# Optimization experiments

Hardware: AMD Instinct MI355X
Metric: run time of the kernel (lower is better)

Reference implementation:

```python
import jax, jax.numpy as jnp
import numpy as np

B, L, D, C, NB = 2, 256, 3, 256, 64
LN_EPS = 1e-5


def setup_inputs() -> dict:
    ks = jax.random.split(jax.random.key(0), 12)
    x_BLD = jax.random.normal(ks[0], (B, L, D), dtype=jnp.float32) * 0.5
    c_BD = jax.random.normal(ks[1], (B, C), dtype=jnp.float32)
    embed_w = jax.random.normal(ks[2], (NB, C), dtype=jnp.float32) * 0.02
    pos_w = jax.random.normal(ks[3], (128, C), dtype=jnp.float32) * 0.02
    bins = jnp.linspace(0.0, 3.0, NB - 1, dtype=jnp.float32)
    ada_w = jax.random.normal(ks[4], (3 * C, C), dtype=jnp.float32) * (C ** -0.5)
    ada_b = jnp.zeros((3 * C,), dtype=jnp.float32)
    ln_g = jnp.ones((C,), dtype=jnp.float32)
    ln_b = jnp.zeros((C,), dtype=jnp.float32)
    fc1_w = jax.random.normal(ks[5], (4 * C, C), dtype=jnp.float32) * (C ** -0.5)
    fc1_b = jnp.zeros((4 * C,), dtype=jnp.float32)
    fc2_w = jax.random.normal(ks[6], (C, 4 * C), dtype=jnp.float32) * ((4 * C) ** -0.5)
    fc2_b = jnp.zeros((C,), dtype=jnp.float32)
    return {"x_BLD": x_BLD, "c_BD": c_BD, "embed_w": embed_w, "pos_w": pos_w,
            "bins": bins, "ada_w": ada_w, "ada_b": ada_b, "ln_g": ln_g,
            "ln_b": ln_b, "fc1_w": fc1_w, "fc1_b": fc1_b, "fc2_w": fc2_w,
            "fc2_b": fc2_b}


def reference(x_BLD, c_BD, embed_w, pos_w, bins, ada_w, ada_b, ln_g, ln_b,
              fc1_w, fc1_b, fc2_w, fc2_b):
    # pairwise squared distances: [B, L, L]
    d_BLL = jnp.sum((x_BLD[:, :, None, :] - x_BLD[:, None, :, :]) ** 2, axis=-1)
    # bucketize (torch.bucketize right=False == searchsorted side='left')
    idx_BLL = jnp.searchsorted(bins, d_BLL, side="left")
    # relative position embedding: [L, L, C]
    rel = jnp.arange(L)[:, None] - jnp.arange(L)[None, :]
    rel = jnp.clip(rel, -64, 63) + 64
    pos_LLD = pos_w[rel]
    # adaLN modulation from conditioning: SiLU -> Linear -> 3 chunks
    mod = jax.nn.silu(c_BD) @ ada_w.T + ada_b            # [B, 3C]
    shift, scale, gate = jnp.split(mod, 3, axis=-1)      # each [B, C]
    shift = shift[:, None, None, :]
    scale = scale[:, None, None, :]
    gate = gate[:, None, None, :]
    # embed + pos, affine modulate
    s = embed_w[idx_BLL] + pos_LLD[None]                 # [B, L, L, C]
    s = s * (1.0 + scale) + shift
    # LayerNorm over channel dim
    mu = jnp.mean(s, axis=-1, keepdims=True)
    var = jnp.mean((s - mu) ** 2, axis=-1, keepdims=True)
    h = (s - mu) * jax.lax.rsqrt(var + LN_EPS) * ln_g + ln_b
    # MLP: Linear -> GELU(exact) -> Linear
    h = jax.nn.gelu(h @ fc1_w.T + fc1_b, approximate=False)
    h = h @ fc2_w.T + fc2_b
    return s + gate * h
```

## Files before the change

### kernel.cpp

```cpp
#include <hip/hip_runtime.h>
#include <math.h>

#define Cn 256
#define Ln 256
#define Bn 2
#define ROWS 8
#define H1 1024
#define NIDX 64
#define NREL 128
#define NCOMBO (Bn * NIDX * NREL)
#define TROWS 32

typedef __attribute__((ext_vector_type(8))) short bf16x8;
typedef __attribute__((ext_vector_type(4))) float f32x4;

__device__ __forceinline__ float gelu_exact(float x) {
    return 0.5f * x * (1.0f + erff(x * 0.70710678118654752f));
}

__device__ __forceinline__ short f2bf(float f) {
    unsigned u = __float_as_uint(f);
    unsigned r = (u + 0x7fffu + ((u >> 16) & 1u)) >> 16;
    return (short)r;
}

__global__ __launch_bounds__(256) void mod_kernel(
    const float* __restrict__ c_BD, const float* __restrict__ ada_w,
    const float* __restrict__ ada_b, float* __restrict__ mod)
{
    int o = blockIdx.x * 256 + threadIdx.x;
    int b = o / (3 * Cn);
    int j = o - b * (3 * Cn);
    const float* crow = c_BD + b * Cn;
    const float* wrow = ada_w + (size_t)j * Cn;
    float acc = 0.f;
    for (int k = 0; k < Cn; k += 4) {
        float4 cv = *(const float4*)(crow + k);
        float4 wv = *(const float4*)(wrow + k);
        acc += (cv.x / (1.f + expf(-cv.x))) * wv.x;
        acc += (cv.y / (1.f + expf(-cv.y))) * wv.y;
        acc += (cv.z / (1.f + expf(-cv.z))) * wv.z;
        acc += (cv.w / (1.f + expf(-cv.w))) * wv.w;
    }
    mod[o] = acc + ada_b[j];
}

__global__ __launch_bounds__(256) void cvt_kernel(
    const float* __restrict__ s, short* __restrict__ d, int n)
{
    int i = (blockIdx.x * 256 + threadIdx.x) * 4;
    if (i < n) {
        float4 v = *(const float4*)(s + i);
        short4 o;
        o.x = f2bf(v.x); o.y = f2bf(v.y); o.z = f2bf(v.z); o.w = f2bf(v.w);
        *(short4*)(d + i) = o;
    }
}

__global__ __launch_bounds__(256) void table_mfma_kernel(
    const float* __restrict__ embed_w, const float* __restrict__ pos_w,
    const float* __restrict__ ln_g, const float* __restrict__ ln_b,
    const short* __restrict__ fc1bf, const float* __restrict__ fc1_b,
    const short* __restrict__ fc2bf, const float* __restrict__ fc2_b,
    const float* __restrict__ mod, float* __restrict__ table)
{
    __shared__ __align__(16) short h_lds[TROWS][264];
    __shared__ __align__(16) short g_lds[TROWS][264];
    __shared__ float s_lds[TROWS][260];

    const int tid  = threadIdx.x;
    const int wave = tid >> 6;
    const int lane = tid & 63;
    const int quad = lane >> 4;
    const int l15  = lane & 15;

    const int base = blockIdx.x * TROWS;
    const int b    = base >> 13;
    const int idx  = (base >> 7) & 63;
    const int rel0 = base & 127;

    const float* modb = mod + b * (3 * Cn);
    const float* erow = embed_w + (size_t)idx * Cn;

    float scale[4], shift[4], lng[4], lnb[4], ev[4];
    #pragma unroll
    for (int m = 0; m < 4; ++m) {
        int c = lane + 64 * m;
        scale[m] = 1.f + modb[Cn + c];
        shift[m] = modb[c];
        lng[m]   = ln_g[c];
        lnb[m]   = ln_b[c];
        ev[m]    = erow[c];
    }

    for (int r8 = 0; r8 < 8; ++r8) {
        const int rr = wave * 8 + r8;
        const float* prow = pos_w + (size_t)(rel0 + rr) * Cn;
        float sv[4]; float sum = 0.f;
        #pragma unroll
        for (int m = 0; m < 4; ++m) {
            float v = (ev[m] + prow[lane + 64 * m]) * scale[m] + shift[m];
            sv[m] = v; sum += v;
        }
        #pragma unroll
        for (int off = 32; off; off >>= 1) sum += __shfl_xor(sum, off, 64);
        float mu = sum * (1.f / Cn);
        float p2 = 0.f;
        #pragma unroll
        for (int m = 0; m < 4; ++m) { float t = sv[m] - mu; p2 += t * t; }
        #pragma unroll
        for (int off = 32; off; off >>= 1) p2 += __shfl_xor(p2, off, 64);
        float rstd = rsqrtf(p2 * (1.f / Cn) + 1e-5f);
        #pragma unroll
        for (int m = 0; m < 4; ++m) {
            int c = lane + 64 * m;
            s_lds[rr][c] = sv[m];
            h_lds[rr][c] = f2bf((sv[m] - mu) * rstd * lng[m] + lnb[m]);
        }
    }
    __syncthreads();

    f32x4 acc2[2][4];
    #pragma unroll
    for (int mt = 0; mt < 2; ++mt)
        #pragma unroll
        for (int nt = 0; nt < 4; ++nt) acc2[mt][nt] = (f32x4){0.f, 0.f, 0.f, 0.f};

    for (int c = 0; c < 4; ++c) {
        f32x4 z[2][4];
        #pragma unroll
        for (int mt = 0; mt < 2; ++mt)
            #pragma unroll
            for (int nt = 0; nt < 4; ++nt) z[mt][nt] = (f32x4){0.f, 0.f, 0.f, 0.f};

        #pragma unroll
        for (int ks = 0; ks < 8; ++ks) {
            int k0 = ks * 32 + quad * 8;
            bf16x8 a0 = *(const bf16x8*)(&h_lds[l15][k0]);
            bf16x8 a1 = *(const bf16x8*)(&h_lds[16 + l15][k0]);
            #pragma unroll
            for (int nt = 0; nt < 4; ++nt) {
                int n = c * 256 + wave * 64 + nt * 16 + l15;
                bf16x8 bf = *(const bf16x8*)(fc1bf + (size_t)n * Cn + k0);
                z[0][nt] = __builtin_amdgcn_mfma_f32_16x16x32_bf16(a0, bf, z[0][nt], 0, 0, 0);
                z[1][nt] = __builtin_amdgcn_mfma_f32_16x16x32_bf16(a1, bf, z[1][nt], 0, 0, 0);
            }
        }
        __syncthreads();
        #pragma unroll
        for (int mt = 0; mt < 2; ++mt)
            #pragma unroll
            for (int nt = 0; nt < 4; ++nt) {
                int coll = wave * 64 + nt * 16 + l15;
                float bias = fc1_b[c * 256 + coll];
                #pragma unroll
                for (int r = 0; r < 4; ++r) {
                    int row = mt * 16 + quad * 4 + r;
                    g_lds[row][coll] = f2bf(gelu_exact(z[mt][nt][r] + bias));
                }
            }
        __syncthreads();
        #pragma unroll
        for (int ks = 0; ks < 8; ++ks) {
            int k0 = ks * 32 + quad * 8;
            bf16x8 a0 = *(const bf16x8*)(&g_lds[l15][k0]);
            bf16x8 a1 = *(const bf16x8*)(&g_lds[16 + l15][k0]);
            #pragma unroll
            for (int nt = 0; nt < 4; ++nt) {
                int n = wave * 64 + nt * 16 + l15;
                bf16x8 bf = *(const bf16x8*)(fc2bf + (size_t)n * H1 + c * 256 + k0);
                acc2[0][nt] = __builtin_amdgcn_mfma_f32_16x16x32_bf16(a0, bf, acc2[0][nt], 0, 0, 0);
                acc2[1][nt] = __builtin_amdgcn_mfma_f32_16x16x32_bf16(a1, bf, acc2[1][nt], 0, 0, 0);
            }
        }
    }

    #pragma unroll
    for (int nt = 0; nt < 4; ++nt) {
        int col = wave * 64 + nt * 16 + l15;
        float bias = fc2_b[col];
        float gate = modb[2 * Cn + col];
        #pragma unroll
        for (int mt = 0; mt < 2; ++mt)
            #pragma unroll
            for (int r = 0; r < 4; ++r) {
                int row = mt * 16 + quad * 4 + r;
                float v = acc2[mt][nt][r] + bias;
                table[(size_t)(base + row) * Cn + col] = s_lds[row][col] + gate * v;
            }
    }
}

__global__ __launch_bounds__(256) void gather_kernel(
    const float* __restrict__ x, const float* __restrict__ bins,
    const float* __restrict__ table, float* __restrict__ out)
{
    __shared__ float xs[Ln * 3];
    __shared__ float bins_s[63];
    __shared__ int   idx_s[64];

    const int tid = threadIdx.x;
    const int blk = blockIdx.x;
    const int q   = blk & 3;
    const int bi  = blk >> 2;
    const int b   = bi >> 8;
    const int i   = bi & 255;

    for (int t = tid; t < Ln * 3; t += 256) xs[t] = x[(size_t)b * Ln * 3 + t];
    if (tid < 63) bins_s[tid] = bins[tid];
    __syncthreads();

    if (tid < 64) {
        int j = q * 64 + tid;
        float d0 = xs[3 * i]     - xs[3 * j];
        float d1 = xs[3 * i + 1] - xs[3 * j + 1];
        float d2 = xs[3 * i + 2] - xs[3 * j + 2];
        float d = d0 * d0 + d1 * d1 + d2 * d2;
        int v = 0;
        #pragma unroll
        for (int k = 0; k < 63; ++k) v += (bins_s[k] < d) ? 1 : 0;
        idx_s[tid] = v;
    }
    __syncthreads();

    const int wave = tid >> 6;
    const int lane = tid & 63;
    float4* outp = (float4*)(out + (size_t)bi * Ln * Cn);
    const float4* tab4 = (const float4*)table;

    #pragma unroll 4
    for (int jj = 0; jj < 16; ++jj) {
        int jl = wave * 16 + jj;
        int j  = q * 64 + jl;
        int idx = idx_s[jl];
        int rel = i - j;
        rel = (rel < -64 ? -64 : (rel > 63 ? 63 : rel)) + 64;
        size_t trow = (size_t)((b * NIDX + idx) * NREL + rel) * (Cn / 4);
        outp[(size_t)j * (Cn / 4) + lane] = tab4[trow + lane];
    }
}

__global__ __launch_bounds__(256) void table_kernel(
    const float* __restrict__ embed_w, const float* __restrict__ pos_w,
    const float* __restrict__ ln_g, const float* __restrict__ ln_b,
    const float* __restrict__ fc1_w, const float* __restrict__ fc1_b,
    const float* __restrict__ fc2_w, const float* __restrict__ fc2_b,
    const float* __restrict__ mod, float* __restrict__ table)
{
    __shared__ float s_tile[ROWS][Cn];
    __shared__ float h_tile[ROWS][Cn];
    __shared__ float g_tile[ROWS][H1];

    const int tid  = threadIdx.x;
    const int wave = tid >> 6;
    const int lane = tid & 63;

    const int base = blockIdx.x * ROWS;
    const int b    = base >> 13;
    const int idx  = (base >> 7) & 63;
    const int rel0 = base & 127;

    const float* modb = mod + b * (3 * Cn);
    const float* erow = embed_w + (size_t)idx * Cn;

    for (int rr = wave; rr < ROWS; rr += 4) {
        const float* prow = pos_w + (size_t)(rel0 + rr) * Cn;
        float sv[4]; float partial = 0.f;
        #pragma unroll
        for (int m = 0; m < 4; ++m) {
            const int c = lane + 64 * m;
            const float v = (erow[c] + prow[c]) * (1.f + modb[Cn + c]) + modb[c];
            sv[m] = v; partial += v;
        }
        float sum = partial;
        #pragma unroll
        for (int off = 32; off; off >>= 1) sum += __shfl_xor(sum, off, 64);
        const float mu = sum * (1.f / Cn);
        float p2 = 0.f;
        #pragma unroll
        for (int m = 0; m < 4; ++m) { const float t = sv[m] - mu; p2 += t * t; }
        float vs = p2;
        #pragma unroll
        for (int off = 32; off; off >>= 1) vs += __shfl_xor(vs, off, 64);
        const float rstd = rsqrtf(vs * (1.f / Cn) + 1e-5f);
        #pragma unroll
        for (int m = 0; m < 4; ++m) {
            const int c = lane + 64 * m;
            s_tile[rr][c] = sv[m];
            h_tile[rr][c] = (sv[m] - mu) * rstd * ln_g[c] + ln_b[c];
        }
    }
    __syncthreads();

    {
        float acc[ROWS][4];
        #pragma unroll
        for (int r = 0; r < ROWS; ++r)
            #pragma unroll
            for (int m = 0; m < 4; ++m) acc[r][m] = 0.f;

        const float* w0 = fc1_w + (size_t)(4 * tid + 0) * Cn;
        const float* w1 = fc1_w + (size_t)(4 * tid + 1) * Cn;
        const float* w2 = fc1_w + (size_t)(4 * tid + 2) * Cn;
        const float* w3 = fc1_w + (size_t)(4 * tid + 3) * Cn;

        for (int k = 0; k < Cn; k += 4) {
            const float4 a0 = *(const float4*)(w0 + k);
            const float4 a1 = *(const float4*)(w1 + k);
            const float4 a2 = *(const float4*)(w2 + k);
            const float4 a3 = *(const float4*)(w3 + k);
            #pragma unroll
            for (int r = 0; r < ROWS; ++r) {
                const float4 h4 = *(const float4*)(&h_tile[r][k]);
                acc[r][0] += h4.x * a0.x + h4.y * a0.y + h4.z * a0.z + h4.w * a0.w;
                acc[r][1] += h4.x * a1.x + h4.y * a1.y + h4.z * a1.z + h4.w * a1.w;
                acc[r][2] += h4.x * a2.x + h4.y * a2.y + h4.z * a2.z + h4.w * a2.w;
                acc[r][3] += h4.x * a3.x + h4.y * a3.y + h4.z * a3.z + h4.w * a3.w;
            }
        }
        const float b0 = fc1_b[4 * tid + 0];
        const float b1 = fc1_b[4 * tid + 1];
        const float b2 = fc1_b[4 * tid + 2];
        const float b3 = fc1_b[4 * tid + 3];
        #pragma unroll
        for (int r = 0; r < ROWS; ++r) {
            float4 g;
            g.x = gelu_exact(acc[r][0] + b0);
            g.y = gelu_exact(acc[r][1] + b1);
            g.z = gelu_exact(acc[r][2] + b2);
            g.w = gelu_exact(acc[r][3] + b3);
            *(float4*)(&g_tile[r][4 * tid]) = g;
        }
    }
    __syncthreads();

    {
        float acc2[ROWS];
        #pragma unroll
        for (int r = 0; r < ROWS; ++r) acc2[r] = 0.f;

        const float* w2r = fc2_w + (size_t)tid * H1;
        for (int k = 0; k < H1; k += 4) {
            const float4 wv = *(const float4*)(w2r + k);
            #pragma unroll
            for (int r = 0; r < ROWS; ++r) {
                const float4 g = *(const float4*)(&g_tile[r][k]);
                acc2[r] += g.x * wv.x + g.y * wv.y + g.z * wv.z + g.w * wv.w;
            }
        }
        const float bias = fc2_b[tid];
        const float gate = modb[2 * Cn + tid];
        #pragma unroll
        for (int r = 0; r < ROWS; ++r)
            table[(size_t)(base + r) * Cn + tid] = s_tile[r][tid] + gate * (acc2[r] + bias);
    }
}

__global__ __launch_bounds__(256) void main_kernel_fb(
    const float* __restrict__ x, const float* __restrict__ embed_w,
    const float* __restrict__ pos_w, const float* __restrict__ bins,
    const float* __restrict__ ln_g, const float* __restrict__ ln_b,
    const float* __restrict__ fc1_w, const float* __restrict__ fc1_b,
    const float* __restrict__ fc2_w, const float* __restrict__ fc2_b,
    const float* __restrict__ mod, float* __restrict__ out)
{
    __shared__ float s_tile[ROWS][Cn];
    __shared__ float h_tile[ROWS][Cn];
    __shared__ float g_tile[ROWS][H1];
    __shared__ float bins_s[64];

    const int tid  = threadIdx.x;
    const int wave = tid >> 6;
    const int lane = tid & 63;

    const long base = (long)blockIdx.x * ROWS;
    const int  b    = (int)(base / (Ln * Ln));
    const int  rem  = (int)(base % (Ln * Ln));
    const int  i    = rem / Ln;
    const int  j0   = rem % Ln;

    if (tid < 63) bins_s[tid] = bins[tid];
    __syncthreads();

    const float* xi = x + ((long)b * Ln + i) * 3;
    const float xi0 = xi[0], xi1 = xi[1], xi2 = xi[2];
    const float* modb = mod + b * (3 * Cn);

    for (int rr = wave; rr < ROWS; rr += 4) {
        const int j = j0 + rr;
        const float* xj = x + ((long)b * Ln + j) * 3;
        const float d0 = xi0 - xj[0], d1 = xi1 - xj[1], d2 = xi2 - xj[2];
        const float d = d0 * d0 + d1 * d1 + d2 * d2;
        int idx = 0;
        #pragma unroll
        for (int k = 0; k < 63; ++k) idx += (bins_s[k] < d) ? 1 : 0;
        int rel = i - j;
        rel = (rel < -64 ? -64 : (rel > 63 ? 63 : rel)) + 64;
        const float* erow = embed_w + (size_t)idx * Cn;
        const float* prow = pos_w + (size_t)rel * Cn;

        float sv[4]; float partial = 0.f;
        #pragma unroll
        for (int m = 0; m < 4; ++m) {
            const int c = lane + 64 * m;
            const float v = (erow[c] + prow[c]) * (1.f + modb[Cn + c]) + modb[c];
            sv[m] = v; partial += v;
        }
        float sum = partial;
        #pragma unroll
        for (int off = 32; off; off >>= 1) sum += __shfl_xor(sum, off, 64);
        const float mu = sum * (1.f / Cn);
        float p2 = 0.f;
        #pragma unroll
        for (int m = 0; m < 4; ++m) { const float t = sv[m] - mu; p2 += t * t; }
        float vs = p2;
        #pragma unroll
        for (int off = 32; off; off >>= 1) vs += __shfl_xor(vs, off, 64);
        const float rstd = rsqrtf(vs * (1.f / Cn) + 1e-5f);
        #pragma unroll
        for (int m = 0; m < 4; ++m) {
            const int c = lane + 64 * m;
            s_tile[rr][c] = sv[m];
            h_tile[rr][c] = (sv[m] - mu) * rstd * ln_g[c] + ln_b[c];
        }
    }
    __syncthreads();

    {
        float acc[ROWS][4];
        #pragma unroll
        for (int r = 0; r < ROWS; ++r)
            #pragma unroll
            for (int m = 0; m < 4; ++m) acc[r][m] = 0.f;

        const float* w0 = fc1_w + (size_t)(4 * tid + 0) * Cn;
        const float* w1 = fc1_w + (size_t)(4 * tid + 1) * Cn;
        const float* w2 = fc1_w + (size_t)(4 * tid + 2) * Cn;
        const float* w3 = fc1_w + (size_t)(4 * tid + 3) * Cn;

        for (int k = 0; k < Cn; k += 4) {
            const float4 a0 = *(const float4*)(w0 + k);
            const float4 a1 = *(const float4*)(w1 + k);
            const float4 a2 = *(const float4*)(w2 + k);
            const float4 a3 = *(const float4*)(w3 + k);
            #pragma unroll
            for (int r = 0; r < ROWS; ++r) {
                const float4 h4 = *(const float4*)(&h_tile[r][k]);
                acc[r][0] += h4.x * a0.x + h4.y * a0.y + h4.z * a0.z + h4.w * a0.w;
                acc[r][1] += h4.x * a1.x + h4.y * a1.y + h4.z * a1.z + h4.w * a1.w;
                acc[r][2] += h4.x * a2.x + h4.y * a2.y + h4.z * a2.z + h4.w * a2.w;
                acc[r][3] += h4.x * a3.x + h4.y * a3.y + h4.z * a3.z + h4.w * a3.w;
            }
        }
        const float b0 = fc1_b[4 * tid + 0];
        const float b1 = fc1_b[4 * tid + 1];
        const float b2 = fc1_b[4 * tid + 2];
        const float b3 = fc1_b[4 * tid + 3];
        #pragma unroll
        for (int r = 0; r < ROWS; ++r) {
            float4 g;
            g.x = gelu_exact(acc[r][0] + b0);
            g.y = gelu_exact(acc[r][1] + b1);
            g.z = gelu_exact(acc[r][2] + b2);
            g.w = gelu_exact(acc[r][3] + b3);
            *(float4*)(&g_tile[r][4 * tid]) = g;
        }
    }
    __syncthreads();

    {
        float acc2[ROWS];
        #pragma unroll
        for (int r = 0; r < ROWS; ++r) acc2[r] = 0.f;

        const float* w2r = fc2_w + (size_t)tid * H1;
        for (int k = 0; k < H1; k += 4) {
            const float4 wv = *(const float4*)(w2r + k);
            #pragma unroll
            for (int r = 0; r < ROWS; ++r) {
                const float4 g = *(const float4*)(&g_tile[r][k]);
                acc2[r] += g.x * wv.x + g.y * wv.y + g.z * wv.z + g.w * wv.w;
            }
        }
        const float bias = fc2_b[tid];
        const float gate = modb[2 * Cn + tid];
        #pragma unroll
        for (int r = 0; r < ROWS; ++r)
            out[(base + r) * Cn + tid] = s_tile[r][tid] + gate * (acc2[r] + bias);
    }
}

extern "C" void kernel_launch(void* const* d_in, const int* in_sizes, int n_in,
                              void* d_out, int out_size, void* d_ws, size_t ws_size,
                              hipStream_t stream) {
    const float* x_BLD   = (const float*)d_in[0];
    const float* c_BD    = (const float*)d_in[1];
    const float* embed_w = (const float*)d_in[2];
    const float* pos_w   = (const float*)d_in[3];
    const float* bins    = (const float*)d_in[4];
    const float* ada_w   = (const float*)d_in[5];
    const float* ada_b   = (const float*)d_in[6];
    const float* ln_g    = (const float*)d_in[7];
    const float* ln_b    = (const float*)d_in[8];
    const float* fc1_w   = (const float*)d_in[9];
    const float* fc1_b   = (const float*)d_in[10];
    const float* fc2_w   = (const float*)d_in[11];
    const float* fc2_b   = (const float*)d_in[12];
    float* out = (float*)d_out;

    float* mod   = (float*)d_ws;
    short* fc1bf = (short*)((char*)d_ws + 8192);
    short* fc2bf = fc1bf + Cn * H1;
    float* table = (float*)((char*)d_ws + 8192 + 2 * Cn * H1 * sizeof(short));

    const size_t need3 = 8192 + 2 * (size_t)Cn * H1 * sizeof(short)
                       + (size_t)NCOMBO * Cn * sizeof(float);
    const size_t need2 = 8192 + (size_t)NCOMBO * Cn * sizeof(float);

    mod_kernel<<<(Bn * 3 * Cn) / 256, 256, 0, stream>>>(c_BD, ada_w, ada_b, mod);

    if (ws_size >= need3) {
        cvt_kernel<<<(Cn * H1 / 4 + 255) / 256, 256, 0, stream>>>(fc1_w, fc1bf, Cn * H1);
        cvt_kernel<<<(Cn * H1 / 4 + 255) / 256, 256, 0, stream>>>(fc2_w, fc2bf, Cn * H1);
        table_mfma_kernel<<<NCOMBO / TROWS, 256, 0, stream>>>(
            embed_w, pos_w, ln_g, ln_b, fc1bf, fc1_b, fc2bf, fc2_b, mod, table);
        gather_kernel<<<Bn * Ln * 4, 256, 0, stream>>>(x_BLD, bins, table, out);
    } else if (ws_size >= need2) {
        float* table2 = (float*)((char*)d_ws + 8192);
        table_kernel<<<NCOMBO / ROWS, 256, 0, stream>>>(
            embed_w, pos_w, ln_g, ln_b, fc1_w, fc1_b, fc2_w, fc2_b, mod, table2);
        gather_kernel<<<Bn * Ln * 4, 256, 0, stream>>>(x_BLD, bins, table2, out);
    } else {
        main_kernel_fb<<<(Bn * Ln * Ln) / ROWS, 256, 0, stream>>>(
            x_BLD, embed_w, pos_w, bins, ln_g, ln_b,
            fc1_w, fc1_b, fc2_w, fc2_b, mod, out);
    }
}
```

Measured before the change: 280.7 us.

## Split table MLP into LN kernel plus two tiled MFMA GEMMs with async LDS loads

Replaces the fused per-32-row table kernel with three stages: a LayerNorm kernel writing bf16 h and fp32 s, a 128x128-tiled bf16 MFMA GEMM for fc1 with fused GELU, and a 64x128-tiled GEMM for fc2 with the fused gate and residual epilogue. Tiles are staged into LDS through global_load_lds async copies, and the gather kernel now issues all 16 loads before its stores. The aim is better weight reuse and MFMA utilisation than the small-row fused kernel. In exchange it writes and reads large intermediate buffers (h, s and the GELU output) through global memory and needs about 76 MB of workspace, falling back to the old fused kernel when less is available.

```diff
diff --git a/kernel.cpp b/kernel.cpp
--- a/kernel.cpp
+++ b/kernel.cpp
@@ -4,24 +4,27 @@
 #define Cn 256
 #define Ln 256
 #define Bn 2
-#define ROWS 8
 #define H1 1024
 #define NIDX 64
 #define NREL 128
-#define NCOMBO (Bn * NIDX * NREL)
+#define NCOMBO 16384
+#define BK 64
 #define TROWS 32
 
 typedef __attribute__((ext_vector_type(8))) short bf16x8;
 typedef __attribute__((ext_vector_type(4))) float f32x4;
+typedef unsigned int u32;
 
 __device__ __forceinline__ float gelu_exact(float x) {
     return 0.5f * x * (1.0f + erff(x * 0.70710678118654752f));
 }
-
 __device__ __forceinline__ short f2bf(float f) {
     unsigned u = __float_as_uint(f);
-    unsigned r = (u + 0x7fffu + ((u >> 16) & 1u)) >> 16;
-    return (short)r;
+    return (short)((u + 0x7fffu + ((u >> 16) & 1u)) >> 16);
+}
+__device__ __forceinline__ void async16(const void* g, void* l) {
+    __builtin_amdgcn_global_load_lds((const __attribute__((address_space(1))) u32*)g,
+                                     (__attribute__((address_space(3))) u32*)l, 16, 0, 0);
 }
 
 __global__ __launch_bounds__(256) void mod_kernel(
@@ -57,6 +60,258 @@
     }
 }
 
+__global__ __launch_bounds__(256) void ln_kernel(
+    const float* __restrict__ embed_w, const float* __restrict__ pos_w,
+    const float* __restrict__ ln_g, const float* __restrict__ ln_b,
+    const float* __restrict__ mod,
+    float* __restrict__ s_out, short* __restrict__ h_out)
+{
+    const int tid  = threadIdx.x;
+    const int wave = tid >> 6;
+    const int lane = tid & 63;
+    const int base = blockIdx.x * 8;
+    const int b    = base >> 13;
+    const int idx  = (base >> 7) & 63;
+    const int rel0 = base & 127;
+    const float* modb = mod + b * (3 * Cn);
+    const int c0 = lane * 4;
+
+    const float4 ev = *(const float4*)(embed_w + (size_t)idx * Cn + c0);
+    const float4 sc = *(const float4*)(modb + Cn + c0);
+    const float4 sh = *(const float4*)(modb + c0);
+    const float4 lg = *(const float4*)(ln_g + c0);
+    const float4 lb = *(const float4*)(ln_b + c0);
+
+    #pragma unroll
+    for (int r8 = 0; r8 < 2; ++r8) {
+        const int rr  = wave * 2 + r8;
+        const int row = base + rr;
+        const float4 p = *(const float4*)(pos_w + (size_t)(rel0 + rr) * Cn + c0);
+        float v0 = (ev.x + p.x) * (1.f + sc.x) + sh.x;
+        float v1 = (ev.y + p.y) * (1.f + sc.y) + sh.y;
+        float v2 = (ev.z + p.z) * (1.f + sc.z) + sh.z;
+        float v3 = (ev.w + p.w) * (1.f + sc.w) + sh.w;
+        float sum = v0 + v1 + v2 + v3;
+        #pragma unroll
+        for (int off = 32; off; off >>= 1) sum += __shfl_xor(sum, off, 64);
+        const float mu = sum * (1.f / Cn);
+        float t0 = v0 - mu, t1 = v1 - mu, t2 = v2 - mu, t3 = v3 - mu;
+        float p2 = t0 * t0 + t1 * t1 + t2 * t2 + t3 * t3;
+        #pragma unroll
+        for (int off = 32; off; off >>= 1) p2 += __shfl_xor(p2, off, 64);
+        const float rstd = rsqrtf(p2 * (1.f / Cn) + 1e-5f);
+
+        *(float4*)(s_out + (size_t)row * Cn + c0) = (float4){v0, v1, v2, v3};
+        short4 hq;
+        hq.x = f2bf(t0 * rstd * lg.x + lb.x);
+        hq.y = f2bf(t1 * rstd * lg.y + lb.y);
+        hq.z = f2bf(t2 * rstd * lg.z + lb.z);
+        hq.w = f2bf(t3 * rstd * lg.w + lb.w);
+        *(short4*)(h_out + (size_t)row * Cn + c0) = hq;
+    }
+}
+
+__global__ __launch_bounds__(256) void gemm1_kernel(
+    const short* __restrict__ h, const short* __restrict__ w1,
+    const float* __restrict__ fc1_b, short* __restrict__ g)
+{
+    __shared__ __align__(16) short Alds[128 * BK];
+    __shared__ __align__(16) short Wlds[128 * BK];
+
+    const int tid  = threadIdx.x;
+    const int wave = tid >> 6;
+    const int lane = tid & 63;
+    const int quad = lane >> 4;
+    const int l15  = lane & 15;
+    const int wm   = wave >> 1, wn = wave & 1;
+    const int m0 = (blockIdx.x >> 3) * 128;
+    const int n0 = (blockIdx.x & 7) * 128;
+
+    const int srow = lane >> 3;
+    const int skel = (lane & 7) * 8;
+
+    f32x4 acc[4][4];
+    #pragma unroll
+    for (int a = 0; a < 4; ++a)
+        #pragma unroll
+        for (int c = 0; c < 4; ++c) acc[a][c] = (f32x4){0.f, 0.f, 0.f, 0.f};
+
+    for (int kt = 0; kt < Cn; kt += BK) {
+        #pragma unroll
+        for (int c = 0; c < 4; ++c) {
+            const int r = wave * 32 + c * 8;
+            async16(h  + (size_t)(m0 + r + srow) * Cn + kt + skel, Alds + r * BK);
+            async16(w1 + (size_t)(n0 + r + srow) * Cn + kt + skel, Wlds + r * BK);
+        }
+        __syncthreads();
+        #pragma unroll
+        for (int ks = 0; ks < 2; ++ks) {
+            bf16x8 wf[4], hf[4];
+            #pragma unroll
+            for (int nt = 0; nt < 4; ++nt)
+                wf[nt] = *(const bf16x8*)(Wlds + (wn * 64 + nt * 16 + l15) * BK + ks * 32 + quad * 8);
+            #pragma unroll
+            for (int mt = 0; mt < 4; ++mt)
+                hf[mt] = *(const bf16x8*)(Alds + (wm * 64 + mt * 16 + l15) * BK + ks * 32 + quad * 8);
+            #pragma unroll
+            for (int mt = 0; mt < 4; ++mt)
+                #pragma unroll
+                for (int nt = 0; nt < 4; ++nt)
+                    acc[mt][nt] = __builtin_amdgcn_mfma_f32_16x16x32_bf16(
+                        wf[nt], hf[mt], acc[mt][nt], 0, 0, 0);
+        }
+        __syncthreads();
+    }
+
+    #pragma unroll
+    for (int mt = 0; mt < 4; ++mt) {
+        const int m = m0 + wm * 64 + mt * 16 + l15;
+        #pragma unroll
+        for (int nt = 0; nt < 4; ++nt) {
+            const int n = n0 + wn * 64 + nt * 16 + quad * 4;
+            const float4 b4 = *(const float4*)(fc1_b + n);
+            short4 o;
+            o.x = f2bf(gelu_exact(acc[mt][nt][0] + b4.x));
+            o.y = f2bf(gelu_exact(acc[mt][nt][1] + b4.y));
+            o.z = f2bf(gelu_exact(acc[mt][nt][2] + b4.z));
+            o.w = f2bf(gelu_exact(acc[mt][nt][3] + b4.w));
+            *(short4*)(g + (size_t)m * H1 + n) = o;
+        }
+    }
+}
+
+__global__ __launch_bounds__(256) void gemm2_kernel(
+    const short* __restrict__ g, const short* __restrict__ w2,
+    const float* __restrict__ fc2_b, const float* __restrict__ s_in,
+    const float* __restrict__ mod, float* __restrict__ table)
+{
+    __shared__ __align__(16) short Alds[64 * BK];
+    __shared__ __align__(16) short Wlds[128 * BK];
+
+    const int tid  = threadIdx.x;
+    const int wave = tid >> 6;
+    const int lane = tid & 63;
+    const int quad = lane >> 4;
+    const int l15  = lane & 15;
+    const int wm   = wave >> 1, wn = wave & 1;
+    const int m0 = (blockIdx.x >> 1) * 64;
+    const int n0 = (blockIdx.x & 1) * 128;
+    const int b  = m0 >> 13;
+    const float* modb = mod + b * (3 * Cn);
+
+    const int srow = lane >> 3;
+    const int skel = (lane & 7) * 8;
+
+    f32x4 acc[2][4];
+    #pragma unroll
+    for (int a = 0; a < 2; ++a)
+        #pragma unroll
+        for (int c = 0; c < 4; ++c) acc[a][c] = (f32x4){0.f, 0.f, 0.f, 0.f};
+
+    for (int kt = 0; kt < H1; kt += BK) {
+        #pragma unroll
+        for (int c = 0; c < 2; ++c) {
+            const int r = wave * 16 + c * 8;
+            async16(g + (size_t)(m0 + r + srow) * H1 + kt + skel, Alds + r * BK);
+        }
+        #pragma unroll
+        for (int c = 0; c < 4; ++c) {
+            const int r = wave * 32 + c * 8;
+            async16(w2 + (size_t)(n0 + r + srow) * H1 + kt + skel, Wlds + r * BK);
+        }
+        __syncthreads();
+        #pragma unroll
+        for (int ks = 0; ks < 2; ++ks) {
+            bf16x8 wf[4], gf[2];
+            #pragma unroll
+            for (int nt = 0; nt < 4; ++nt)
+                wf[nt] = *(const bf16x8*)(Wlds + (wn * 64 + nt * 16 + l15) * BK + ks * 32 + quad * 8);
+            #pragma unroll
+            for (int mt = 0; mt < 2; ++mt)
+                gf[mt] = *(const bf16x8*)(Alds + (wm * 32 + mt * 16 + l15) * BK + ks * 32 + quad * 8);
+            #pragma unroll
+            for (int mt = 0; mt < 2; ++mt)
+                #pragma unroll
+                for (int nt = 0; nt < 4; ++nt)
+                    acc[mt][nt] = __builtin_amdgcn_mfma_f32_16x16x32_bf16(
+                        wf[nt], gf[mt], acc[mt][nt], 0, 0, 0);
+        }
+        __syncthreads();
+    }
+
+    #pragma unroll
+    for (int mt = 0; mt < 2; ++mt) {
+        const int m = m0 + wm * 32 + mt * 16 + l15;
+        #pragma unroll
+        for (int nt = 0; nt < 4; ++nt) {
+            const int n = n0 + wn * 64 + nt * 16 + quad * 4;
+            const float4 b4 = *(const float4*)(fc2_b + n);
+            const float4 g4 = *(const float4*)(modb + 2 * Cn + n);
+            const float4 s4 = *(const float4*)(s_in + (size_t)m * Cn + n);
+            float4 o;
+            o.x = s4.x + g4.x * (acc[mt][nt][0] + b4.x);
+            o.y = s4.y + g4.y * (acc[mt][nt][1] + b4.y);
+            o.z = s4.z + g4.z * (acc[mt][nt][2] + b4.z);
+            o.w = s4.w + g4.w * (acc[mt][nt][3] + b4.w);
+            *(float4*)(table + (size_t)m * Cn + n) = o;
+        }
+    }
+}
+
+__global__ __launch_bounds__(256) void gather_kernel(
+    const float* __restrict__ x, const float* __restrict__ bins,
+    const float* __restrict__ table, float* __restrict__ out)
+{
+    __shared__ float xs[Ln * 3];
+    __shared__ float bins_s[63];
+    __shared__ int   idx_s[64];
+
+    const int tid = threadIdx.x;
+    const int blk = blockIdx.x;
+    const int q   = blk & 3;
+    const int bi  = blk >> 2;
+    const int b   = bi >> 8;
+    const int i   = bi & 255;
+
+    for (int t = tid; t < Ln * 3; t += 256) xs[t] = x[(size_t)b * Ln * 3 + t];
+    if (tid < 63) bins_s[tid] = bins[tid];
+    __syncthreads();
+
+    if (tid < 64) {
+        int j = q * 64 + tid;
+        float d0 = xs[3 * i]     - xs[3 * j];
+        float d1 = xs[3 * i + 1] - xs[3 * j + 1];
+        float d2 = xs[3 * i + 2] - xs[3 * j + 2];
+        float d = d0 * d0 + d1 * d1 + d2 * d2;
+        int v = 0;
+        #pragma unroll
+        for (int k = 0; k < 63; ++k) v += (bins_s[k] < d) ? 1 : 0;
+        idx_s[tid] = v;
+    }
+    __syncthreads();
+
+    const int wave = tid >> 6;
+    const int lane = tid & 63;
+    float4* outp = (float4*)(out + (size_t)bi * Ln * Cn);
+    const float4* tab4 = (const float4*)table;
+
+    float4 v[16];
+    #pragma unroll
+    for (int jj = 0; jj < 16; ++jj) {
+        int jl  = wave * 16 + jj;
+        int j   = q * 64 + jl;
+        int rel = i - j;
+        rel = (rel < -64 ? -64 : (rel > 63 ? 63 : rel)) + 64;
+        size_t trow = (size_t)((b * NIDX + idx_s[jl]) * NREL + rel) * (Cn / 4);
+        v[jj] = tab4[trow + lane];
+    }
+    #pragma unroll
+    for (int jj = 0; jj < 16; ++jj) {
+        int j = q * 64 + wave * 16 + jj;
+        outp[(size_t)j * (Cn / 4) + lane] = v[jj];
+    }
+}
+
 __global__ __launch_bounds__(256) void table_mfma_kernel(
     const float* __restrict__ embed_w, const float* __restrict__ pos_w,
     const float* __restrict__ ln_g, const float* __restrict__ ln_b,
@@ -188,305 +443,6 @@
                 float v = acc2[mt][nt][r] + bias;
                 table[(size_t)(base + row) * Cn + col] = s_lds[row][col] + gate * v;
             }
-    }
-}
-
-__global__ __launch_bounds__(256) void gather_kernel(
-    const float* __restrict__ x, const float* __restrict__ bins,
-    const float* __restrict__ table, float* __restrict__ out)
-{
-    __shared__ float xs[Ln * 3];
-    __shared__ float bins_s[63];
-    __shared__ int   idx_s[64];
-
-    const int tid = threadIdx.x;
-    const int blk = blockIdx.x;
-    const int q   = blk & 3;
-    const int bi  = blk >> 2;
-    const int b   = bi >> 8;
-    const int i   = bi & 255;
-
-    for (int t = tid; t < Ln * 3; t += 256) xs[t] = x[(size_t)b * Ln * 3 + t];
-    if (tid < 63) bins_s[tid] = bins[tid];
-    __syncthreads();
-
-    if (tid < 64) {
-        int j = q * 64 + tid;
-        float d0 = xs[3 * i]     - xs[3 * j];
-        float d1 = xs[3 * i + 1] - xs[3 * j + 1];
-        float d2 = xs[3 * i + 2] - xs[3 * j + 2];
-        float d = d0 * d0 + d1 * d1 + d2 * d2;
-        int v = 0;
-        #pragma unroll
-        for (int k = 0; k < 63; ++k) v += (bins_s[k] < d) ? 1 : 0;
-        idx_s[tid] = v;
-    }
-    __syncthreads();
-
-    const int wave = tid >> 6;
-    const int lane = tid & 63;
-    float4* outp = (float4*)(out + (size_t)bi * Ln * Cn);
-    const float4* tab4 = (const float4*)table;
-
-    #pragma unroll 4
-    for (int jj = 0; jj < 16; ++jj) {
-        int jl = wave * 16 + jj;
-        int j  = q * 64 + jl;
-        int idx = idx_s[jl];
-        int rel = i - j;
-        rel = (rel < -64 ? -64 : (rel > 63 ? 63 : rel)) + 64;
-        size_t trow = (size_t)((b * NIDX + idx) * NREL + rel) * (Cn / 4);
-        outp[(size_t)j * (Cn / 4) + lane] = tab4[trow + lane];
-    }
-}
-
-__global__ __launch_bounds__(256) void table_kernel(
-    const float* __restrict__ embed_w, const float* __restrict__ pos_w,
-    const float* __restrict__ ln_g, const float* __restrict__ ln_b,
-    const float* __restrict__ fc1_w, const float* __restrict__ fc1_b,
-    const float* __restrict__ fc2_w, const float* __restrict__ fc2_b,
-    const float* __restrict__ mod, float* __restrict__ table)
-{
-    __shared__ float s_tile[ROWS][Cn];
-    __shared__ float h_tile[ROWS][Cn];
-    __shared__ float g_tile[ROWS][H1];
-
-    const int tid  = threadIdx.x;
-    const int wave = tid >> 6;
-    const int lane = tid & 63;
-
-    const int base = blockIdx.x * ROWS;
-    const int b    = base >> 13;
-    const int idx  = (base >> 7) & 63;
-    const int rel0 = base & 127;
-
-    const float* modb = mod + b * (3 * Cn);
-    const float* erow = embed_w + (size_t)idx * Cn;
-
-    for (int rr = wave; rr < ROWS; rr += 4) {
-        const float* prow = pos_w + (size_t)(rel0 + rr) * Cn;
-        float sv[4]; float partial = 0.f;
-        #pragma unroll
-        for (int m = 0; m < 4; ++m) {
-            const int c = lane + 64 * m;
-            const float v = (erow[c] + prow[c]) * (1.f + modb[Cn + c]) + modb[c];
-            sv[m] = v; partial += v;
-        }
-        float sum = partial;
-        #pragma unroll
-        for (int off = 32; off; off >>= 1) sum += __shfl_xor(sum, off, 64);
-        const float mu = sum * (1.f / Cn);
-        float p2 = 0.f;
-        #pragma unroll
-        for (int m = 0; m < 4; ++m) { const float t = sv[m] - mu; p2 += t * t; }
-        float vs = p2;
-        #pragma unroll
-        for (int off = 32; off; off >>= 1) vs += __shfl_xor(vs, off, 64);
-        const float rstd = rsqrtf(vs * (1.f / Cn) + 1e-5f);
-        #pragma unroll
-        for (int m = 0; m < 4; ++m) {
-            const int c = lane + 64 * m;
-            s_tile[rr][c] = sv[m];
-            h_tile[rr][c] = (sv[m] - mu) * rstd * ln_g[c] + ln_b[c];
-        }
-    }
-    __syncthreads();
-
-    {
-        float acc[ROWS][4];
-        #pragma unroll
-        for (int r = 0; r < ROWS; ++r)
-            #pragma unroll
-            for (int m = 0; m < 4; ++m) acc[r][m] = 0.f;
-
-        const float* w0 = fc1_w + (size_t)(4 * tid + 0) * Cn;
-        const float* w1 = fc1_w + (size_t)(4 * tid + 1) * Cn;
-        const float* w2 = fc1_w + (size_t)(4 * tid + 2) * Cn;
-        const float* w3 = fc1_w + (size_t)(4 * tid + 3) * Cn;
-
-        for (int k = 0; k < Cn; k += 4) {
-            const float4 a0 = *(const float4*)(w0 + k);
-            const float4 a1 = *(const float4*)(w1 + k);
-            const float4 a2 = *(const float4*)(w2 + k);
-            const float4 a3 = *(const float4*)(w3 + k);
-            #pragma unroll
-            for (int r = 0; r < ROWS; ++r) {
-                const float4 h4 = *(const float4*)(&h_tile[r][k]);
-                acc[r][0] += h4.x * a0.x + h4.y * a0.y + h4.z * a0.z + h4.w * a0.w;
-                acc[r][1] += h4.x * a1.x + h4.y * a1.y + h4.z * a1.z + h4.w * a1.w;
-                acc[r][2] += h4.x * a2.x + h4.y * a2.y + h4.z * a2.z + h4.w * a2.w;
-                acc[r][3] += h4.x * a3.x + h4.y * a3.y + h4.z * a3.z + h4.w * a3.w;
-            }
-        }
-        const float b0 = fc1_b[4 * tid + 0];
-        const float b1 = fc1_b[4 * tid + 1];
-        const float b2 = fc1_b[4 * tid + 2];
-        const float b3 = fc1_b[4 * tid + 3];
-        #pragma unroll
-        for (int r = 0; r < ROWS; ++r) {
-            float4 g;
-            g.x = gelu_exact(acc[r][0] + b0);
-            g.y = gelu_exact(acc[r][1] + b1);
-            g.z = gelu_exact(acc[r][2] + b2);
-            g.w = gelu_exact(acc[r][3] + b3);
-            *(float4*)(&g_tile[r][4 * tid]) = g;
-        }
-    }
-    __syncthreads();
-
-    {
-        float acc2[ROWS];
-        #pragma unroll
-        for (int r = 0; r < ROWS; ++r) acc2[r] = 0.f;
-
-        const float* w2r = fc2_w + (size_t)tid * H1;
-        for (int k = 0; k < H1; k += 4) {
-            const float4 wv = *(const float4*)(w2r + k);
-            #pragma unroll
-            for (int r = 0; r < ROWS; ++r) {
-                const float4 g = *(const float4*)(&g_tile[r][k]);
-                acc2[r] += g.x * wv.x + g.y * wv.y + g.z * wv.z + g.w * wv.w;
-            }
-        }
-        const float bias = fc2_b[tid];
-        const float gate = modb[2 * Cn + tid];
-        #pragma unroll
-        for (int r = 0; r < ROWS; ++r)
-            table[(size_t)(base + r) * Cn + tid] = s_tile[r][tid] + gate * (acc2[r] + bias);
-    }
-}
-
-__global__ __launch_bounds__(256) void main_kernel_fb(
-    const float* __restrict__ x, const float* __restrict__ embed_w,
-    const float* __restrict__ pos_w, const float* __restrict__ bins,
-    const float* __restrict__ ln_g, const float* __restrict__ ln_b,
-    const float* __restrict__ fc1_w, const float* __restrict__ fc1_b,
-    const float* __restrict__ fc2_w, const float* __restrict__ fc2_b,
-    const float* __restrict__ mod, float* __restrict__ out)
-{
-    __shared__ float s_tile[ROWS][Cn];
-    __shared__ float h_tile[ROWS][Cn];
-    __shared__ float g_tile[ROWS][H1];
-    __shared__ float bins_s[64];
-
-    const int tid  = threadIdx.x;
-    const int wave = tid >> 6;
-    const int lane = tid & 63;
-
-    const long base = (long)blockIdx.x * ROWS;
-    const int  b    = (int)(base / (Ln * Ln));
-    const int  rem  = (int)(base % (Ln * Ln));
-    const int  i    = rem / Ln;
-    const int  j0   = rem % Ln;
-
-    if (tid < 63) bins_s[tid] = bins[tid];
-    __syncthreads();
-
-    const float* xi = x + ((long)b * Ln + i) * 3;
-    const float xi0 = xi[0], xi1 = xi[1], xi2 = xi[2];
-    const float* modb = mod + b * (3 * Cn);
-
-    for (int rr = wave; rr < ROWS; rr += 4) {
-        const int j = j0 + rr;
-        const float* xj = x + ((long)b * Ln + j) * 3;
-        const float d0 = xi0 - xj[0], d1 = xi1 - xj[1], d2 = xi2 - xj[2];
-        const float d = d0 * d0 + d1 * d1 + d2 * d2;
-        int idx = 0;
-        #pragma unroll
-        for (int k = 0; k < 63; ++k) idx += (bins_s[k] < d) ? 1 : 0;
-        int rel = i - j;
-        rel = (rel < -64 ? -64 : (rel > 63 ? 63 : rel)) + 64;
-        const float* erow = embed_w + (size_t)idx * Cn;
-        const float* prow = pos_w + (size_t)rel * Cn;
-
-        float sv[4]; float partial = 0.f;
-        #pragma unroll
-        for (int m = 0; m < 4; ++m) {
-            const int c = lane + 64 * m;
-            const float v = (erow[c] + prow[c]) * (1.f + modb[Cn + c]) + modb[c];
-            sv[m] = v; partial += v;
-        }
-        float sum = partial;
-        #pragma unroll
-        for (int off = 32; off; off >>= 1) sum += __shfl_xor(sum, off, 64);
-        const float mu = sum * (1.f / Cn);
-        float p2 = 0.f;
-        #pragma unroll
-        for (int m = 0; m < 4; ++m) { const float t = sv[m] - mu; p2 += t * t; }
-        float vs = p2;
-        #pragma unroll
-        for (int off = 32; off; off >>= 1) vs += __shfl_xor(vs, off, 64);
-        const float rstd = rsqrtf(vs * (1.f / Cn) + 1e-5f);
-        #pragma unroll
-        for (int m = 0; m < 4; ++m) {
-            const int c = lane + 64 * m;
-            s_tile[rr][c] = sv[m];
-            h_tile[rr][c] = (sv[m] - mu) * rstd * ln_g[c] + ln_b[c];
-        }
-    }
-    __syncthreads();
-
-    {
-        float acc[ROWS][4];
-        #pragma unroll
-        for (int r = 0; r < ROWS; ++r)
-            #pragma unroll
-            for (int m = 0; m < 4; ++m) acc[r][m] = 0.f;
-
-        const float* w0 = fc1_w + (size_t)(4 * tid + 0) * Cn;
-        const float* w1 = fc1_w + (size_t)(4 * tid + 1) * Cn;
-        const float* w2 = fc1_w + (size_t)(4 * tid + 2) * Cn;
-        const float* w3 = fc1_w + (size_t)(4 * tid + 3) * Cn;
-
-        for (int k = 0; k < Cn; k += 4) {
-            const float4 a0 = *(const float4*)(w0 + k);
-            const float4 a1 = *(const float4*)(w1 + k);
-            const float4 a2 = *(const float4*)(w2 + k);
-            const float4 a3 = *(const float4*)(w3 + k);
-            #pragma unroll
-            for (int r = 0; r < ROWS; ++r) {
-                const float4 h4 = *(const float4*)(&h_tile[r][k]);
-                acc[r][0] += h4.x * a0.x + h4.y * a0.y + h4.z * a0.z + h4.w * a0.w;
-                acc[r][1] += h4.x * a1.x + h4.y * a1.y + h4.z * a1.z + h4.w * a1.w;
-                acc[r][2] += h4.x * a2.x + h4.y * a2.y + h4.z * a2.z + h4.w * a2.w;
-                acc[r][3] += h4.x * a3.x + h4.y * a3.y + h4.z * a3.z + h4.w * a3.w;
-            }
-        }
-        const float b0 = fc1_b[4 * tid + 0];
-        const float b1 = fc1_b[4 * tid + 1];
-        const float b2 = fc1_b[4 * tid + 2];
-        const float b3 = fc1_b[4 * tid + 3];
-        #pragma unroll
-        for (int r = 0; r < ROWS; ++r) {
-            float4 g;
-            g.x = gelu_exact(acc[r][0] + b0);
-            g.y = gelu_exact(acc[r][1] + b1);
-            g.z = gelu_exact(acc[r][2] + b2);
-            g.w = gelu_exact(acc[r][3] + b3);
-            *(float4*)(&g_tile[r][4 * tid]) = g;
-        }
-    }
-    __syncthreads();
-
-    {
-        float acc2[ROWS];
-        #pragma unroll
-        for (int r = 0; r < ROWS; ++r) acc2[r] = 0.f;
-
-        const float* w2r = fc2_w + (size_t)tid * H1;
-        for (int k = 0; k < H1; k += 4) {
-            const float4 wv = *(const float4*)(w2r + k);
-            #pragma unroll
-            for (int r = 0; r < ROWS; ++r) {
-                const float4 g = *(const float4*)(&g_tile[r][k]);
-                acc2[r] += g.x * wv.x + g.y * wv.y + g.z * wv.z + g.w * wv.w;
-            }
-        }
-        const float bias = fc2_b[tid];
-        const float gate = modb[2 * Cn + tid];
-        #pragma unroll
-        for (int r = 0; r < ROWS; ++r)
-            out[(base + r) * Cn + tid] = s_tile[r][tid] + gate * (acc2[r] + bias);
     }
 }
 
@@ -508,31 +464,35 @@
     const float* fc2_b   = (const float*)d_in[12];
     float* out = (float*)d_out;
 
-    float* mod   = (float*)d_ws;
-    short* fc1bf = (short*)((char*)d_ws + 8192);
-    short* fc2bf = fc1bf + Cn * H1;
-    float* table = (float*)((char*)d_ws + 8192 + 2 * Cn * H1 * sizeof(short));
-
-    const size_t need3 = 8192 + 2 * (size_t)Cn * H1 * sizeof(short)
+    char* ws = (char*)d_ws;
+    float* mod   = (float*)ws;
+    short* fc1bf = (short*)(ws + 8192);
+    short* fc2bf = (short*)(ws + 8192 + 524288);
+    short* hbuf  = (short*)(ws + 1056768);
+    float* sbuf  = (float*)(ws + 9445376);
+    short* gbuf  = (short*)(ws + 26222592);
+    float* tableA= (float*)(ws + 59777024);
+    const size_t needA = 76554240;
+    const size_t needB = 8192 + 2 * (size_t)Cn * H1 * sizeof(short)
                        + (size_t)NCOMBO * Cn * sizeof(float);
-    const size_t need2 = 8192 + (size_t)NCOMBO * Cn * sizeof(float);
 
     mod_kernel<<<(Bn * 3 * Cn) / 256, 256, 0, stream>>>(c_BD, ada_w, ada_b, mod);
-
-    if (ws_size >= need3) {
-        cvt_kernel<<<(Cn * H1 / 4 + 255) / 256, 256, 0, stream>>>(fc1_w, fc1bf, Cn * H1);
-        cvt_kernel<<<(Cn * H1 / 4 + 255) / 256, 256, 0, stream>>>(fc2_w, fc2bf, Cn * H1);
+    cvt_kernel<<<(Cn * H1 / 4 + 255) / 256, 256, 0, stream>>>(fc1_w, fc1bf, Cn * H1);
+    cvt_kernel<<<(Cn * H1 / 4 + 255) / 256, 256, 0, stream>>>(fc2_w, fc2bf, Cn * H1);
+
+    if (ws_size >= needA) {
+        ln_kernel<<<NCOMBO / 8, 256, 0, stream>>>(
+            embed_w, pos_w, ln_g, ln_b, mod, sbuf, hbuf);
+        gemm1_kernel<<<(NCOMBO / 128) * (H1 / 128), 256, 0, stream>>>(
+            hbuf, fc1bf, fc1_b, gbuf);
+        gemm2_kernel<<<(NCOMBO / 64) * (Cn / 128), 256, 0, stream>>>(
+            gbuf, fc2bf, fc2_b, sbuf, mod, tableA);
+        gather_kernel<<<Bn * Ln * 4, 256, 0, stream>>>(x_BLD, bins, tableA, out);
+    } else {
+        float* tableB = (float*)(ws + 8192 + 2 * (size_t)Cn * H1 * sizeof(short));
+        (void)needB;
         table_mfma_kernel<<<NCOMBO / TROWS, 256, 0, stream>>>(
-            embed_w, pos_w, ln_g, ln_b, fc1bf, fc1_b, fc2bf, fc2_b, mod, table);
-        gather_kernel<<<Bn * Ln * 4, 256, 0, stream>>>(x_BLD, bins, table, out);
-    } else if (ws_size >= need2) {
-        float* table2 = (float*)((char*)d_ws + 8192);
-        table_kernel<<<NCOMBO / ROWS, 256, 0, stream>>>(
-            embed_w, pos_w, ln_g, ln_b, fc1_w, fc1_b, fc2_w, fc2_b, mod, table2);
-        gather_kernel<<<Bn * Ln * 4, 256, 0, stream>>>(x_BLD, bins, table2, out);
-    } else {
-        main_kernel_fb<<<(Bn * Ln * Ln) / ROWS, 256, 0, stream>>>(
-            x_BLD, embed_w, pos_w, bins, ln_g, ln_b,
-            fc1_w, fc1_b, fc2_w, fc2_b, mod, out);
-    }
-}
+            embed_w, pos_w, ln_g, ln_b, fc1bf, fc1_b, fc2bf, fc2_b, mod, tableB);
+        gather_kernel<<<Bn * Ln * 4, 256, 0, stream>>>(x_BLD, bins, tableB, out);
+    }
+}
```

New measurement: 255.7 us. 8.9% less time.
